# Optimization experiments

Hardware: AMD Instinct MI355X
Metric: run time of the kernel (lower is better)

Reference implementation:

```python
import jax, jax.numpy as jnp
import numpy as np

B, S, D = 2, 2048, 2048
H, KVH, HD = 16, 4, 128
I = 8192
EPS = 1e-6
SCALE = HD ** -0.5
NEG = -1e9


def rms_norm(x, w):
    xf = x.astype(jnp.float32)
    var = jnp.mean(xf * xf, axis=-1, keepdims=True)
    return (w * (xf * jax.lax.rsqrt(var + EPS)).astype(x.dtype))


def rope(x, cos_f, sin_f):
    # x: (B, h, S, HD); cos_f/sin_f: (B, 1, S, HD//2). Interleaved pairs.
    xp = x.reshape(*x.shape[:-1], HD // 2, 2)
    xr, xi = xp[..., 0], xp[..., 1]
    rr = cos_f * xr - sin_f * xi
    ri = sin_f * xr + cos_f * xi
    return jnp.stack([rr, ri], axis=-1).reshape(x.shape)


def setup_inputs() -> dict:
    key = jax.random.key(0)
    ks = jax.random.split(key, 12)
    inp = {
        "hidden_states": jax.random.normal(ks[0], (B, S, D), jnp.float32),
        "cos": jax.random.normal(ks[1], (B, S, HD), jnp.float32),
        "sin": jax.random.normal(ks[2], (B, S, HD), jnp.float32),
    }
    # additive causal mask (B,1,S,S)
    causal = jnp.tril(jnp.ones((S, S), jnp.bool_))
    inp["attention_mask"] = jnp.where(causal, 0.0, NEG).astype(jnp.float32)[None, None].repeat(B, 0)
    sc = 0.02
    inp["wq"] = jax.random.normal(ks[3], (H * HD, D), jnp.float32) * sc
    inp["wk"] = jax.random.normal(ks[4], (KVH * HD, D), jnp.float32) * sc
    inp["wv"] = jax.random.normal(ks[5], (KVH * HD, D), jnp.float32) * sc
    inp["wo"] = jax.random.normal(ks[6], (D, H * HD), jnp.float32) * sc
    inp["w_gate"] = jax.random.normal(ks[7], (I, D), jnp.float32) * sc
    inp["w_up"] = jax.random.normal(ks[8], (I, D), jnp.float32) * sc
    inp["w_down"] = jax.random.normal(ks[9], (D, I), jnp.float32) * sc
    inp["ln1_w"] = jnp.ones((D,), jnp.float32)
    inp["ln2_w"] = jnp.ones((D,), jnp.float32)
    return inp


def layer_fwd(hidden_states, cos, sin, attention_mask,
              wq, wk, wv, wo, w_gate, w_up, w_down, ln1_w, ln2_w):
    residual = hidden_states
    h = rms_norm(hidden_states, ln1_w)
    # projections
    q = jnp.einsum('bsd,ed->bse', h, wq).reshape(B, S, H, HD).transpose(0, 2, 1, 3)
    k = jnp.einsum('bsd,ed->bse', h, wk).reshape(B, S, KVH, HD).transpose(0, 2, 1, 3)
    v = jnp.einsum('bsd,ed->bse', h, wv).reshape(B, S, KVH, HD).transpose(0, 2, 1, 3)
    cos_f = cos[..., :HD // 2][:, None]  # (B,1,S,HD/2)
    sin_f = sin[..., :HD // 2][:, None]
    q = rope(q, cos_f, sin_f)
    k = rope(k, cos_f, sin_f)
    # GQA: repeat_interleave kv heads
    n_rep = H // KVH
    k = jnp.repeat(k, n_rep, axis=1)
    v = jnp.repeat(v, n_rep, axis=1)
    scores = jnp.einsum('bhqd,bhkd->bhqk', q, k) * SCALE + attention_mask
    probs = jax.nn.softmax(scores.astype(jnp.float32), axis=-1).astype(q.dtype)
    attn = jnp.einsum('bhqk,bhkd->bhqd', probs, v)
    attn = attn.transpose(0, 2, 1, 3).reshape(B, S, H * HD)
    attn_out = jnp.einsum('bse,de->bsd', attn, wo)
    h = residual + attn_out
    residual = h
    m = rms_norm(h, ln2_w)
    gate = jax.nn.silu(jnp.einsum('bsd,id->bsi', m, w_gate))
    up = jnp.einsum('bsd,id->bsi', m, w_up)
    mlp_out = jnp.einsum('bsi,di->bsd', gate * up, w_down)
    return residual + mlp_out


def reference(hidden_states, cos, sin, attention_mask,
              wq, wk, wv, wo, w_gate, w_up, w_down, ln1_w, ln2_w):
    return layer_fwd(hidden_states, cos, sin, attention_mask,
                     wq, wk, wv, wo, w_gate, w_up, w_down, ln1_w, ln2_w)
```

## Files before the change

### kernel.cpp

```cpp
#include <hip/hip_runtime.h>
#include <cstdint>
#include <cstddef>

typedef unsigned short u16;
typedef short bf16x8 __attribute__((ext_vector_type(8)));
typedef float floatx4 __attribute__((ext_vector_type(4)));

__device__ __forceinline__ float b2f(u16 u) {
    union { unsigned int i; float f; } v; v.i = ((unsigned int)u) << 16; return v.f;
}
__device__ __forceinline__ u16 f2b(float f) {
    union { float f; unsigned int i; } v; v.f = f;
    unsigned int u = v.i;
    unsigned int r = (u + 0x7fffu + ((u >> 16) & 1u)) >> 16;
    return (u16)r;
}

#define GLL16(gptr, lptr)                                                          \
    __builtin_amdgcn_global_load_lds(                                              \
        (__attribute__((address_space(1))) void*)(gptr),                           \
        (__attribute__((address_space(3))) void*)(lptr), 16, 0, 0)

#define BAR_LGKM() asm volatile("s_waitcnt lgkmcnt(0)\n\ts_barrier" ::: "memory")
#define WAIT_VM8_BAR() asm volatile("s_waitcnt vmcnt(8)\n\ts_barrier" ::: "memory")
#define WAIT_VM0_BAR() asm volatile("s_waitcnt vmcnt(0)\n\ts_barrier" ::: "memory")
#define WAITV_BAR(n) asm volatile("s_waitcnt vmcnt(" #n ")\n\ts_barrier" ::: "memory")

__global__ __launch_bounds__(256) void cvt_all(
    const float* __restrict__ wq, const float* __restrict__ wk,
    const float* __restrict__ wvp, const float* __restrict__ wo,
    const float* __restrict__ wg, const float* __restrict__ wu,
    const float* __restrict__ wd,
    u16* __restrict__ wqkv, u16* __restrict__ wob, u16* __restrict__ wgb,
    u16* __restrict__ wub, u16* __restrict__ wdb) {
    long v = (long)blockIdx.x * 256 + threadIdx.x;
    const float* s; u16* d; long o;
    if (v < 1048576)       { s = wq;  d = wqkv;           o = v; }
    else if (v < 1310720)  { s = wk;  d = wqkv + 4194304; o = v - 1048576; }
    else if (v < 1572864)  { s = wvp; d = wqkv + 5242880; o = v - 1310720; }
    else if (v < 2621440)  { s = wo;  d = wob;            o = v - 1572864; }
    else if (v < 6815744)  { s = wg;  d = wgb;            o = v - 2621440; }
    else if (v < 11010048) { s = wu;  d = wub;            o = v - 6815744; }
    else                   { s = wd;  d = wdb;            o = v - 11010048; }
    float4 x = ((const float4*)s)[o];
    u16 t[4] = { f2b(x.x), f2b(x.y), f2b(x.z), f2b(x.w) };
    ((ushort4*)d)[o] = *(const ushort4*)t;
}

__global__ __launch_bounds__(256) void rmsnorm_kernel(const float* __restrict__ x,
                                                      const float* __restrict__ w,
                                                      u16* __restrict__ out) {
    __shared__ float red[4];
    const int row = blockIdx.x;
    const float* xr = x + (size_t)row * 2048;
    const int d0 = threadIdx.x * 8;
    float4 a = *(const float4*)&xr[d0];
    float4 b = *(const float4*)&xr[d0 + 4];
    float s = a.x*a.x + a.y*a.y + a.z*a.z + a.w*a.w +
              b.x*b.x + b.y*b.y + b.z*b.z + b.w*b.w;
    #pragma unroll
    for (int m = 1; m < 64; m <<= 1) s += __shfl_xor(s, m);
    const int lane = threadIdx.x & 63, wv = threadIdx.x >> 6;
    if (lane == 0) red[wv] = s;
    __syncthreads();
    float tot = red[0] + red[1] + red[2] + red[3];
    float r = rsqrtf(tot * (1.0f / 2048.0f) + 1e-6f);
    const float* wp = w + d0;
    u16 o[8];
    o[0] = f2b(a.x * r * wp[0]); o[1] = f2b(a.y * r * wp[1]);
    o[2] = f2b(a.z * r * wp[2]); o[3] = f2b(a.w * r * wp[3]);
    o[4] = f2b(b.x * r * wp[4]); o[5] = f2b(b.y * r * wp[5]);
    o[6] = f2b(b.z * r * wp[6]); o[7] = f2b(b.w * r * wp[7]);
    *(bf16x8*)&out[(size_t)row * 2048 + d0] = *(const bf16x8*)o;
}

__global__ __launch_bounds__(256, 2) void gemm_bt(
    const u16* __restrict__ A, const u16* __restrict__ W,
    int M, int N, int K, int mode,
    u16* __restrict__ outb, float* __restrict__ outf,
    const float* __restrict__ res) {

    __shared__ __align__(16) u16 smA[2][128 * 64];
    __shared__ __align__(16) u16 smB[2][128 * 64];

    const int tid  = threadIdx.x;
    const int lane = tid & 63;
    const int c    = lane & 15;
    const int quad = lane >> 4;
    const int wv   = tid >> 6;
    const int wm   = (wv >> 1) * 64;
    const int wn   = (wv & 1) * 64;
    const int row0 = blockIdx.y * 128;
    const int col0 = blockIdx.x * 128;

    const u16* aB[4]; const u16* bB[4]; int lo[4];
    #pragma unroll
    for (int p = 0; p < 4; ++p) {
        int lin = p * 256 + tid, r = lin >> 3, g = lin & 7, sg = g ^ (r & 7);
        aB[p] = A + (size_t)(row0 + r) * K + sg * 8;
        bB[p] = W + (size_t)(col0 + r) * K + sg * 8;
        lo[p] = lin * 8;
    }
    #pragma unroll
    for (int p = 0; p < 4; ++p) { GLL16(aB[p], &smA[0][lo[p]]); GLL16(bB[p], &smB[0][lo[p]]); }

    floatx4 acc[4][4] = {};
    const int nk = K >> 6;
    for (int k = 0; k < nk; ++k) {
        BAR_LGKM();
        if (k + 1 < nk) {
            const int nb = (k + 1) & 1, ko = (k + 1) << 6;
            #pragma unroll
            for (int p = 0; p < 4; ++p) {
                GLL16(aB[p] + ko, &smA[nb][lo[p]]);
                GLL16(bB[p] + ko, &smB[nb][lo[p]]);
            }
            WAIT_VM8_BAR();
        } else {
            WAIT_VM0_BAR();
        }
        const u16* sA = smA[k & 1];
        const u16* sB = smB[k & 1];
        #pragma unroll
        for (int ks = 0; ks < 2; ++ks) {
            bf16x8 af[4], bfr[4];
            #pragma unroll
            for (int mi = 0; mi < 4; ++mi) {
                int r = wm + mi * 16 + c;
                int pos = (ks * 4 + quad) ^ (c & 7);
                af[mi] = *(const bf16x8*)&sA[r * 64 + pos * 8];
            }
            #pragma unroll
            for (int ni = 0; ni < 4; ++ni) {
                int r = wn + ni * 16 + c;
                int pos = (ks * 4 + quad) ^ (c & 7);
                bfr[ni] = *(const bf16x8*)&sB[r * 64 + pos * 8];
            }
            #pragma unroll
            for (int mi = 0; mi < 4; ++mi)
                #pragma unroll
                for (int ni = 0; ni < 4; ++ni)
                    acc[mi][ni] = __builtin_amdgcn_mfma_f32_16x16x32_bf16(
                        af[mi], bfr[ni], acc[mi][ni], 0, 0, 0);
        }
    }

    #pragma unroll
    for (int mi = 0; mi < 4; ++mi) {
        #pragma unroll
        for (int r = 0; r < 4; ++r) {
            int row = row0 + wm + mi * 16 + quad * 4 + r;
            #pragma unroll
            for (int ni = 0; ni < 4; ++ni) {
                int col = col0 + wn + ni * 16 + c;
                size_t idx = (size_t)row * N + col;
                float v = acc[mi][ni][r];
                if (mode == 0) outb[idx] = f2b(v);
                else           outf[idx] = v + res[idx];
            }
        }
    }
}

#define STAGE_G(buf, ko) { GLL16(gSrc0 + (ko), &smG[buf][guD0]); GLL16(gSrc1 + (ko), &smG[buf][guD1]); }
#define STAGE_U(buf, ko) { GLL16(uSrc0 + (ko), &smU[buf][guD0]); GLL16(uSrc1 + (ko), &smU[buf][guD1]); }
#define STAGE_A2(buf, ko, j0, j1)                                              \
    { GLL16(aSrc + (size_t)(j0) * 32 * 2048 + (ko), &smA[buf][aDst + (j0) * 32 * 64]); \
      GLL16(aSrc + (size_t)(j1) * 32 * 2048 + (ko), &smA[buf][aDst + (j1) * 32 * 64]); }

#define MLP_PHASE(ph, STAGE_STMT, WAIT_STMT)                                   \
    {                                                                          \
        bf16x8 af[2][2];                                                       \
        _Pragma("unroll")                                                      \
        for (int mi = 0; mi < 2; ++mi)                                         \
            _Pragma("unroll")                                                  \
            for (int ks = 0; ks < 2; ++ks) {                                   \
                int r = wm + (ph) * 32 + mi * 16 + c;                          \
                int pos = (ks * 4 + quad) ^ (c & 7);                           \
                af[mi][ks] = *(const bf16x8*)&sA[r * 64 + pos * 8];            \
            }                                                                  \
        STAGE_STMT;                                                            \
        __builtin_amdgcn_s_barrier();                                          \
        asm volatile("s_waitcnt lgkmcnt(0)" ::: "memory");                     \
        __builtin_amdgcn_s_setprio(1);                                         \
        _Pragma("unroll")                                                      \
        for (int mi = 0; mi < 2; ++mi)                                         \
            _Pragma("unroll")                                                  \
            for (int ks = 0; ks < 2; ++ks)                                     \
                _Pragma("unroll")                                              \
                for (int ni = 0; ni < 2; ++ni) {                               \
                    ag[(ph) * 2 + mi][ni] = __builtin_amdgcn_mfma_f32_16x16x32_bf16( \
                        af[mi][ks], bg[ni][ks], ag[(ph) * 2 + mi][ni], 0, 0, 0);     \
                    au[(ph) * 2 + mi][ni] = __builtin_amdgcn_mfma_f32_16x16x32_bf16( \
                        af[mi][ks], bu[ni][ks], au[(ph) * 2 + mi][ni], 0, 0, 0);     \
                }                                                              \
        __builtin_amdgcn_s_setprio(0);                                         \
        WAIT_STMT;                                                             \
    }

__global__ __launch_bounds__(512, 2) void mlp_gateup3(
    const u16* __restrict__ A, const u16* __restrict__ Wg,
    const u16* __restrict__ Wu, u16* __restrict__ out) {

    __shared__ __align__(16) u16 smA[2][256 * 64];
    __shared__ __align__(16) u16 smG[2][128 * 64];
    __shared__ __align__(16) u16 smU[2][128 * 64];

    const int K = 2048;
    const int tid  = threadIdx.x;
    const int lane = tid & 63;
    const int c    = lane & 15;
    const int quad = lane >> 4;
    const int wv   = tid >> 6;
    const int wm   = (wv >> 2) * 128;
    const int wn   = (wv & 3) * 32;
    const int row0 = blockIdx.y * 256;
    const int col0 = blockIdx.x * 128;

    const int rloc = tid >> 3, g = tid & 7;
    const int Rbase = (tid < 256) ? rloc : (96 + rloc);
    const int sgA = g ^ (rloc & 7);
    const u16* aSrc = A + (size_t)(row0 + Rbase) * K + sgA * 8;
    const int aDst = Rbase * 64 + g * 8;

    const u16* gSrc0; const u16* gSrc1; const u16* uSrc0; const u16* uSrc1;
    int guD0, guD1;
    {
        int lin = tid, r = lin >> 3, gg = lin & 7, sg = gg ^ (r & 7);
        gSrc0 = Wg + (size_t)(col0 + r) * K + sg * 8;
        uSrc0 = Wu + (size_t)(col0 + r) * K + sg * 8;
        guD0 = lin * 8;
        lin = 512 + tid; r = lin >> 3; gg = lin & 7; sg = gg ^ (r & 7);
        gSrc1 = Wg + (size_t)(col0 + r) * K + sg * 8;
        uSrc1 = Wu + (size_t)(col0 + r) * K + sg * 8;
        guD1 = lin * 8;
    }

    STAGE_G(0, 0); STAGE_U(0, 0); STAGE_A2(0, 0, 0, 1); STAGE_A2(0, 0, 2, 3);
    WAITV_BAR(3);

    floatx4 ag[8][2] = {}, au[8][2] = {};
    const int nk = K >> 6;
    for (int k = 0; k < nk; ++k) {
        const int cur = k & 1, nb = cur ^ 1;
        const int ko = (k + 1) << 6;
        const u16* sA = smA[cur];
        const u16* sG = smG[cur];
        const u16* sU = smU[cur];

        bf16x8 bg[2][2], bu[2][2];
        #pragma unroll
        for (int ks = 0; ks < 2; ++ks)
            #pragma unroll
            for (int ni = 0; ni < 2; ++ni) {
                int r = wn + ni * 16 + c;
                int pos = (ks * 4 + quad) ^ (c & 7);
                bg[ni][ks] = *(const bf16x8*)&sG[r * 64 + pos * 8];
                bu[ni][ks] = *(const bf16x8*)&sU[r * 64 + pos * 8];
            }

        if (k + 1 < nk) {
            MLP_PHASE(0, STAGE_G(nb, ko),        WAITV_BAR(4));
            MLP_PHASE(1, STAGE_U(nb, ko),        WAITV_BAR(5));
            MLP_PHASE(2, STAGE_A2(nb, ko, 0, 1), WAITV_BAR(6));
            MLP_PHASE(3, STAGE_A2(nb, ko, 2, 3), WAITV_BAR(3));
        } else {
            MLP_PHASE(0, , WAITV_BAR(2));
            MLP_PHASE(1, , WAITV_BAR(1));
            MLP_PHASE(2, , WAITV_BAR(0));
            MLP_PHASE(3, , );
        }
    }

    #pragma unroll
    for (int mi = 0; mi < 8; ++mi) {
        #pragma unroll
        for (int r = 0; r < 4; ++r) {
            int row = row0 + wm + mi * 16 + quad * 4 + r;
            #pragma unroll
            for (int ni = 0; ni < 2; ++ni) {
                int col = col0 + wn + ni * 16 + c;
                float gv = ag[mi][ni][r];
                float uv = au[mi][ni][r];
                float sg_ = gv / (1.0f + __expf(-gv));
                out[(size_t)row * 8192 + col] = f2b(sg_ * uv);
            }
        }
    }
}

__global__ __launch_bounds__(256) void rope_kernel(u16* __restrict__ qkv,
                                                   const float* __restrict__ cs,
                                                   const float* __restrict__ sn) {
    const int t = blockIdx.x;
    const int hh = blockIdx.y * 4 + (threadIdx.x >> 6);
    const int j = threadIdx.x & 63;
    size_t base = (size_t)t * 3072 + (hh < 16 ? hh * 128 : 2048 + (hh - 16) * 128);
    float cf = cs[(size_t)t * 128 + j];
    float sf = sn[(size_t)t * 128 + j];
    ushort2 xv = *(ushort2*)&qkv[base + 2 * j];
    float xr = b2f(xv.x), xi = b2f(xv.y);
    ushort2 ov;
    ov.x = f2b(cf * xr - sf * xi);
    ov.y = f2b(sf * xr + cf * xi);
    *(ushort2*)&qkv[base + 2 * j] = ov;
}

__global__ __launch_bounds__(256) void transpose_v(const u16* __restrict__ qkv,
                                                   u16* __restrict__ vt) {
    __shared__ __align__(16) u16 T[64][136];
    const int bkv = blockIdx.x;
    const int st = blockIdx.y;
    const int b = bkv >> 2, kvh = bkv & 3;
    const int tid = threadIdx.x;
    #pragma unroll
    for (int it = 0; it < 4; ++it) {
        int lin = it * 256 + tid;
        int sr = lin >> 4, gr = lin & 15;
        bf16x8 v = *(const bf16x8*)&qkv[((size_t)(b * 2048 + st * 64 + sr)) * 3072 +
                                        2560 + kvh * 128 + gr * 8];
        *(bf16x8*)&T[sr][gr * 8] = v;
    }
    __syncthreads();
    #pragma unroll
    for (int it = 0; it < 4; ++it) {
        int lin = it * 256 + tid;
        int n = lin >> 3, sc = lin & 7;
        u16 tmp[8];
        #pragma unroll
        for (int j = 0; j < 8; ++j) tmp[j] = T[sc * 8 + j][n];
        *(bf16x8*)&vt[((size_t)(bkv * 128 + n)) * 2048 + st * 64 + sc * 8] =
            *(const bf16x8*)tmp;
    }
}

__global__ __launch_bounds__(256, 2) void attn_kernel(const u16* __restrict__ qkv,
                                                      const u16* __restrict__ vt,
                                                      u16* __restrict__ attnb) {
    __shared__ __align__(16) u16 sK[64 * 128];
    __shared__ __align__(16) u16 sV[128 * 64];
    __shared__ __align__(16) u16 sP[4][16 * 80];

    const int tid  = threadIdx.x;
    const int lane = tid & 63;
    const int c    = lane & 15;
    const int quad = lane >> 4;
    const int wv   = tid >> 6;

    const int qt  = 31 - (int)blockIdx.x;
    const int bh  = blockIdx.y;
    const int b   = bh >> 4;
    const int h   = bh & 15;
    const int kvh = h >> 2;

    const int qrow = qt * 64 + wv * 16 + c;
    const size_t qbase = ((size_t)(b * 2048 + qrow)) * 3072 + h * 128;
    bf16x8 qf[4];
    #pragma unroll
    for (int kk = 0; kk < 4; ++kk)
        qf[kk] = *(const bf16x8*)&qkv[qbase + kk * 32 + quad * 8];

    floatx4 o[8] = {};
    float m_[4], l_[4];
    #pragma unroll
    for (int r = 0; r < 4; ++r) { m_[r] = -__builtin_inff(); l_[r] = 0.0f; }

    const float SC = 0.08838834764831845f;

    for (int kt = 0; kt <= qt; ++kt) {
        const int kv0 = kt * 64;
        __syncthreads();
        #pragma unroll
        for (int p = 0; p < 4; ++p) {
            int lin = p * 256 + tid;
            {
                int r = lin >> 4, g = lin & 15;
                int sg = g ^ (r & 7);
                const u16* gk = qkv + ((size_t)(b * 2048 + kv0 + r)) * 3072 +
                                2048 + kvh * 128 + sg * 8;
                GLL16(gk, &sK[lin * 8]);
            }
            {
                int r = lin >> 3, g = lin & 7;
                int sg = g ^ (r & 7);
                const u16* gv = vt + ((size_t)((b * 4 + kvh) * 128 + r)) * 2048 +
                                kv0 + sg * 8;
                GLL16(gv, &sV[lin * 8]);
            }
        }
        __syncthreads();

        floatx4 s[4] = {};
        #pragma unroll
        for (int kk = 0; kk < 4; ++kk) {
            #pragma unroll
            for (int ct = 0; ct < 4; ++ct) {
                int rk = ct * 16 + c;
                int pos = (kk * 4 + quad) ^ (c & 7);
                bf16x8 kf = *(const bf16x8*)&sK[rk * 128 + pos * 8];
                s[ct] = __builtin_amdgcn_mfma_f32_16x16x32_bf16(qf[kk], kf, s[ct], 0, 0, 0);
            }
        }

        const int qloc = wv * 16 + quad * 4;
        #pragma unroll
        for (int ct = 0; ct < 4; ++ct) {
            #pragma unroll
            for (int r = 0; r < 4; ++r) {
                float v = s[ct][r] * SC;
                if (kt == qt && (ct * 16 + c) > (qloc + r)) v = -__builtin_inff();
                s[ct][r] = v;
            }
        }

        float alpha[4];
        #pragma unroll
        for (int r = 0; r < 4; ++r) {
            float rm = fmaxf(fmaxf(s[0][r], s[1][r]), fmaxf(s[2][r], s[3][r]));
            rm = fmaxf(rm, __shfl_xor(rm, 1));
            rm = fmaxf(rm, __shfl_xor(rm, 2));
            rm = fmaxf(rm, __shfl_xor(rm, 4));
            rm = fmaxf(rm, __shfl_xor(rm, 8));
            float mn = fmaxf(m_[r], rm);
            alpha[r] = __expf(m_[r] - mn);
            m_[r] = mn;
        }
        #pragma unroll
        for (int r = 0; r < 4; ++r) {
            float rs = 0.0f;
            #pragma unroll
            for (int ct = 0; ct < 4; ++ct) {
                float p = __expf(s[ct][r] - m_[r]);
                s[ct][r] = p;
                rs += p;
            }
            rs += __shfl_xor(rs, 1);
            rs += __shfl_xor(rs, 2);
            rs += __shfl_xor(rs, 4);
            rs += __shfl_xor(rs, 8);
            l_[r] = l_[r] * alpha[r] + rs;
        }

        u16* sp = &sP[wv][0];
        #pragma unroll
        for (int ct = 0; ct < 4; ++ct)
            #pragma unroll
            for (int r = 0; r < 4; ++r)
                sp[(quad * 4 + r) * 80 + ct * 16 + c] = f2b(s[ct][r]);

        #pragma unroll
        for (int nt = 0; nt < 8; ++nt)
            #pragma unroll
            for (int r = 0; r < 4; ++r)
                o[nt][r] *= alpha[r];

        #pragma unroll
        for (int ks2 = 0; ks2 < 2; ++ks2) {
            bf16x8 pa = *(const bf16x8*)&sp[c * 80 + ks2 * 32 + quad * 8];
            #pragma unroll
            for (int nt = 0; nt < 8; ++nt) {
                int rv = nt * 16 + c;
                int pos = (ks2 * 4 + quad) ^ (c & 7);
                bf16x8 vb = *(const bf16x8*)&sV[rv * 64 + pos * 8];
                o[nt] = __builtin_amdgcn_mfma_f32_16x16x32_bf16(pa, vb, o[nt], 0, 0, 0);
            }
        }
    }

    float inv[4];
    #pragma unroll
    for (int r = 0; r < 4; ++r) inv[r] = 1.0f / l_[r];
    #pragma unroll
    for (int nt = 0; nt < 8; ++nt) {
        #pragma unroll
        for (int r = 0; r < 4; ++r) {
            int row = qt * 64 + wv * 16 + quad * 4 + r;
            int col = h * 128 + nt * 16 + c;
            attnb[((size_t)(b * 2048 + row)) * 2048 + col] = f2b(o[nt][r] * inv[r]);
        }
    }
}

extern "C" void kernel_launch(void* const* d_in, const int* in_sizes, int n_in,
                              void* d_out, int out_size, void* d_ws, size_t ws_size,
                              hipStream_t stream) {
    const float* hidden = (const float*)d_in[0];
    const float* cosp   = (const float*)d_in[1];
    const float* sinp   = (const float*)d_in[2];
    const float* wq  = (const float*)d_in[4];
    const float* wk  = (const float*)d_in[5];
    const float* wvp = (const float*)d_in[6];
    const float* wo  = (const float*)d_in[7];
    const float* wg  = (const float*)d_in[8];
    const float* wu  = (const float*)d_in[9];
    const float* wd  = (const float*)d_in[10];
    const float* ln1 = (const float*)d_in[11];
    const float* ln2 = (const float*)d_in[12];
    float* outp = (float*)d_out;

    char* ws = (char*)d_ws;
    size_t off = 0;
    auto alloc = [&](size_t bytes) {
        void* p = ws + off;
        off += (bytes + 255) & ~(size_t)255;
        return p;
    };
    u16* wqkv_b  = (u16*)alloc((size_t)3072 * 2048 * 2);
    u16* wo_b    = (u16*)alloc((size_t)2048 * 2048 * 2);
    u16* wg_b    = (u16*)alloc((size_t)8192 * 2048 * 2);
    u16* wu_b    = (u16*)alloc((size_t)8192 * 2048 * 2);
    u16* wd_b    = (u16*)alloc((size_t)2048 * 8192 * 2);
    u16* normed  = (u16*)alloc((size_t)4096 * 2048 * 2);
    u16* qkv     = (u16*)alloc((size_t)4096 * 3072 * 2);
    u16* vtb     = (u16*)alloc((size_t)8 * 128 * 2048 * 2);
    u16* attnb   = (u16*)alloc((size_t)4096 * 2048 * 2);
    float* h1    = (float*)alloc((size_t)4096 * 2048 * 4);
    u16* hidprod = (u16*)alloc((size_t)4096 * 8192 * 2);
    (void)ws_size; (void)in_sizes; (void)n_in; (void)out_size;

    cvt_all<<<59392, 256, 0, stream>>>(wq, wk, wvp, wo, wg, wu, wd,
                                       wqkv_b, wo_b, wg_b, wu_b, wd_b);

    rmsnorm_kernel<<<4096, 256, 0, stream>>>(hidden, ln1, normed);

    gemm_bt<<<dim3(24, 32), 256, 0, stream>>>(normed, wqkv_b, 4096, 3072, 2048, 0,
                                              qkv, nullptr, nullptr);

    rope_kernel<<<dim3(4096, 5), 256, 0, stream>>>(qkv, cosp, sinp);
    transpose_v<<<dim3(8, 32), 256, 0, stream>>>(qkv, vtb);
    attn_kernel<<<dim3(32, 32), 256, 0, stream>>>(qkv, vtb, attnb);

    gemm_bt<<<dim3(16, 32), 256, 0, stream>>>(attnb, wo_b, 4096, 2048, 2048, 1,
                                              nullptr, h1, hidden);

    rmsnorm_kernel<<<4096, 256, 0, stream>>>(h1, ln2, normed);

    mlp_gateup3<<<dim3(64, 16), 512, 0, stream>>>(normed, wg_b, wu_b, hidprod);

    gemm_bt<<<dim3(16, 32), 256, 0, stream>>>(hidprod, wd_b, 4096, 2048, 8192, 1,
                                              nullptr, outp, h1);
}
```

Measured before the change: 1.085 ms.

## Restage gate/up MLP GEMM pipeline and remap blocks across XCDs

Reworks the fused gate/up GEMM kernel's load pipeline. The first phase now issues the G, U and first A chunk together, and the remaining A chunks are spread across later phases. Each vmcnt wait and barrier moves to the start of its phase, with B-fragment reads happening after that barrier. The grid is also flattened to 1D and block IDs are remapped so that blocks landing on the same XCD share row and column tiles, which is meant to improve L2 reuse. The aim is better overlap of global-to-LDS loads with MFMA and better cache locality, at the cost of subtle wait-count correctness risks.

```diff
diff --git a/kernel.cpp b/kernel.cpp
--- a/kernel.cpp
+++ b/kernel.cpp
@@ -24,7 +24,8 @@
 #define BAR_LGKM() asm volatile("s_waitcnt lgkmcnt(0)\n\ts_barrier" ::: "memory")
 #define WAIT_VM8_BAR() asm volatile("s_waitcnt vmcnt(8)\n\ts_barrier" ::: "memory")
 #define WAIT_VM0_BAR() asm volatile("s_waitcnt vmcnt(0)\n\ts_barrier" ::: "memory")
-#define WAITV_BAR(n) asm volatile("s_waitcnt vmcnt(" #n ")\n\ts_barrier" ::: "memory")
+#define VMW(n) asm volatile("s_waitcnt vmcnt(" #n ")" ::: "memory")
+#define LGKM0() asm volatile("s_waitcnt lgkmcnt(0)" ::: "memory")
 
 __global__ __launch_bounds__(256) void cvt_all(
     const float* __restrict__ wq, const float* __restrict__ wk,
@@ -164,12 +165,25 @@
 
 #define STAGE_G(buf, ko) { GLL16(gSrc0 + (ko), &smG[buf][guD0]); GLL16(gSrc1 + (ko), &smG[buf][guD1]); }
 #define STAGE_U(buf, ko) { GLL16(uSrc0 + (ko), &smU[buf][guD0]); GLL16(uSrc1 + (ko), &smU[buf][guD1]); }
-#define STAGE_A2(buf, ko, j0, j1)                                              \
-    { GLL16(aSrc + (size_t)(j0) * 32 * 2048 + (ko), &smA[buf][aDst + (j0) * 32 * 64]); \
-      GLL16(aSrc + (size_t)(j1) * 32 * 2048 + (ko), &smA[buf][aDst + (j1) * 32 * 64]); }
-
-#define MLP_PHASE(ph, STAGE_STMT, WAIT_STMT)                                   \
+#define STAGE_A(buf, ko, j)                                                    \
+    GLL16(aSrc + (size_t)(j) * 32 * 2048 + (ko), &smA[buf][aDst + (j) * 32 * 64])
+
+#define READ_B()                                                               \
+    _Pragma("unroll")                                                          \
+    for (int ks = 0; ks < 2; ++ks)                                             \
+        _Pragma("unroll")                                                      \
+        for (int ni = 0; ni < 2; ++ni) {                                       \
+            int r = wn + ni * 16 + c;                                          \
+            int pos = (ks * 4 + quad) ^ (c & 7);                               \
+            bg[ni][ks] = *(const bf16x8*)&sG[r * 64 + pos * 8];                \
+            bu[ni][ks] = *(const bf16x8*)&sU[r * 64 + pos * 8];                \
+        }
+
+#define MLP_PH(ph, WAITCODE, READS_EXTRA, STAGE_STMT)                          \
     {                                                                          \
+        WAITCODE;                                                              \
+        __builtin_amdgcn_s_barrier();                                          \
+        READS_EXTRA;                                                           \
         bf16x8 af[2][2];                                                       \
         _Pragma("unroll")                                                      \
         for (int mi = 0; mi < 2; ++mi)                                         \
@@ -180,8 +194,7 @@
                 af[mi][ks] = *(const bf16x8*)&sA[r * 64 + pos * 8];            \
             }                                                                  \
         STAGE_STMT;                                                            \
-        __builtin_amdgcn_s_barrier();                                          \
-        asm volatile("s_waitcnt lgkmcnt(0)" ::: "memory");                     \
+        LGKM0();                                                               \
         __builtin_amdgcn_s_setprio(1);                                         \
         _Pragma("unroll")                                                      \
         for (int mi = 0; mi < 2; ++mi)                                         \
@@ -195,10 +208,9 @@
                         af[mi][ks], bu[ni][ks], au[(ph) * 2 + mi][ni], 0, 0, 0);     \
                 }                                                              \
         __builtin_amdgcn_s_setprio(0);                                         \
-        WAIT_STMT;                                                             \
-    }
-
-__global__ __launch_bounds__(512, 2) void mlp_gateup3(
+    }
+
+__global__ __launch_bounds__(512, 2) void mlp_gateup4(
     const u16* __restrict__ A, const u16* __restrict__ Wg,
     const u16* __restrict__ Wu, u16* __restrict__ out) {
 
@@ -214,8 +226,11 @@
     const int wv   = tid >> 6;
     const int wm   = (wv >> 2) * 128;
     const int wn   = (wv & 3) * 32;
-    const int row0 = blockIdx.y * 256;
-    const int col0 = blockIdx.x * 128;
+
+    const int bid  = (int)blockIdx.x;
+    const int orig = (bid & 7) * 128 + (bid >> 3);
+    const int row0 = (orig & 15) * 256;
+    const int col0 = (orig >> 4) * 128;
 
     const int rloc = tid >> 3, g = tid & 7;
     const int Rbase = (tid < 256) ? rloc : (96 + rloc);
@@ -236,8 +251,8 @@
         guD1 = lin * 8;
     }
 
-    STAGE_G(0, 0); STAGE_U(0, 0); STAGE_A2(0, 0, 0, 1); STAGE_A2(0, 0, 2, 3);
-    WAITV_BAR(3);
+    STAGE_G(0, 0); STAGE_U(0, 0);
+    STAGE_A(0, 0, 0); STAGE_A(0, 0, 1); STAGE_A(0, 0, 2); STAGE_A(0, 0, 3);
 
     floatx4 ag[8][2] = {}, au[8][2] = {};
     const int nk = K >> 6;
@@ -247,28 +262,19 @@
         const u16* sA = smA[cur];
         const u16* sG = smG[cur];
         const u16* sU = smU[cur];
-
         bf16x8 bg[2][2], bu[2][2];
-        #pragma unroll
-        for (int ks = 0; ks < 2; ++ks)
-            #pragma unroll
-            for (int ni = 0; ni < 2; ++ni) {
-                int r = wn + ni * 16 + c;
-                int pos = (ks * 4 + quad) ^ (c & 7);
-                bg[ni][ks] = *(const bf16x8*)&sG[r * 64 + pos * 8];
-                bu[ni][ks] = *(const bf16x8*)&sU[r * 64 + pos * 8];
-            }
 
         if (k + 1 < nk) {
-            MLP_PHASE(0, STAGE_G(nb, ko),        WAITV_BAR(4));
-            MLP_PHASE(1, STAGE_U(nb, ko),        WAITV_BAR(5));
-            MLP_PHASE(2, STAGE_A2(nb, ko, 0, 1), WAITV_BAR(6));
-            MLP_PHASE(3, STAGE_A2(nb, ko, 2, 3), WAITV_BAR(3));
+            MLP_PH(0, VMW(3), READ_B(),
+                   { STAGE_G(nb, ko); STAGE_U(nb, ko); STAGE_A(nb, ko, 0); });
+            MLP_PH(1, VMW(7), , STAGE_A(nb, ko, 1));
+            MLP_PH(2, VMW(7), , STAGE_A(nb, ko, 2));
+            MLP_PH(3, VMW(7), , STAGE_A(nb, ko, 3));
         } else {
-            MLP_PHASE(0, , WAITV_BAR(2));
-            MLP_PHASE(1, , WAITV_BAR(1));
-            MLP_PHASE(2, , WAITV_BAR(0));
-            MLP_PHASE(3, , );
+            MLP_PH(0, VMW(3), READ_B(), );
+            MLP_PH(1, VMW(2), , );
+            MLP_PH(2, VMW(1), , );
+            MLP_PH(3, VMW(0), , );
         }
     }
 
@@ -535,7 +541,7 @@
 
     rmsnorm_kernel<<<4096, 256, 0, stream>>>(h1, ln2, normed);
 
-    mlp_gateup3<<<dim3(64, 16), 512, 0, stream>>>(normed, wg_b, wu_b, hidprod);
+    mlp_gateup4<<<dim3(1024), 512, 0, stream>>>(normed, wg_b, wu_b, hidprod);
 
     gemm_bt<<<dim3(16, 32), 256, 0, stream>>>(hidprod, wd_b, 4096, 2048, 8192, 1,
                                               nullptr, outp, h1);
```

Measured after the change: 1.068 ms. No clear change (-1.5%).
